# Performance work log

Measured on AMD Instinct MI355X. Metric: run time of the kernel, lower is better.

## Reference

```python
import jax, jax.numpy as jnp
import numpy as np

EPS = 1e-5
GROUPS = 32


def conv1x1(x, W, b):
    # x: (B,C,T), W: (O,C), b: (O,)
    return jnp.einsum('bct,oc->bot', x, W) + b[None, :, None]


def group_norm(x, gamma, beta):
    B, C, T = x.shape
    xg = x.reshape(B, GROUPS, (C // GROUPS) * T)
    mu = xg.mean(axis=-1, keepdims=True)
    var = xg.var(axis=-1, keepdims=True)
    xn = ((xg - mu) * jax.lax.rsqrt(var + EPS)).reshape(B, C, T)
    return xn * gamma[None, :, None] + beta[None, :, None]


def block(x, W, b, gamma, beta):
    return jax.nn.relu(group_norm(conv1x1(x, W, b), gamma, beta))


def setup_inputs() -> dict:
    key = jax.random.key(0)
    ks = jax.random.split(key, 8)
    B, C, P, T, TF = 4, 512, 512, 2048, 4096
    inp = {
        'feature': jax.random.normal(ks[0], (B, C, T), jnp.float32),
        'frame_level_feature': jax.random.uniform(ks[1], (B, C, TF), jnp.float32),
        # cur_point_conv: conv1x1 C->P + GN(32,P)
        'W1': jax.random.normal(ks[2], (P, C), jnp.float32) / np.sqrt(C),
        'b1': jnp.zeros((P,), jnp.float32),
        'g1': jnp.ones((P,), jnp.float32),
        'be1': jnp.zeros((P,), jnp.float32),
        # lr_conv: conv1x1 C->2P + GN(32,2P)
        'W2': jax.random.normal(ks[3], (2 * P, C), jnp.float32) / np.sqrt(C),
        'b2': jnp.zeros((2 * P,), jnp.float32),
        'g2': jnp.ones((2 * P,), jnp.float32),
        'be2': jnp.zeros((2 * P,), jnp.float32),
        # proposal_conv: conv1x1 4P->C + GN(32,C)
        'W3': jax.random.normal(ks[4], (C, 4 * P), jnp.float32) / np.sqrt(4 * P),
        'b3': jnp.zeros((C,), jnp.float32),
        'g3': jnp.ones((C,), jnp.float32),
        'be3': jnp.zeros((C,), jnp.float32),
    }
    return inp


def reference(feature, frame_level_feature, W1, b1, g1, be1, W2, b2, g2, be2, W3, b3, g3, be3):
    fm_short = block(feature, W1, b1, g1, be1)          # (B,P,T)
    feat = block(feature, W2, b2, g2, be2)              # (B,2P,T)
    t = feature.shape[2]
    # inverse-CDF resampling (uses batch 0 statistics, as original)
    mean_values = frame_level_feature.mean(axis=1)[0]   # (TF,)
    mean_values = mean_values / mean_values.sum()
    cdf = (jnp.cumsum(mean_values) * t).astype(jnp.int32)
    cdf = jnp.minimum(cdf, t - 1)                       # (TF,)
    # exact vectorization of findNearNum loop: first index with minimal |cdf-i|
    targets = jnp.arange(t, dtype=jnp.int32)
    idx = jnp.argmin(jnp.abs(cdf[None, :] - targets[:, None]), axis=1)  # (t,)
    sampled = frame_level_feature[:, :, idx]            # (B,C,t)
    mixed = jnp.concatenate([sampled, feat, fm_short], axis=1)  # (B,4P,t)
    mixed = block(mixed, W3, b3, g3, be3)               # (B,C,t)
    return (mixed, feat)
```

## Files before the change

kernel.cpp:

```cpp
#include <hip/hip_runtime.h>

typedef unsigned short u16;
typedef unsigned int   u32;
typedef __attribute__((ext_vector_type(8))) short short8;
typedef __attribute__((ext_vector_type(4))) short short4_t;
typedef __attribute__((ext_vector_type(4))) float f32x4;

__device__ __forceinline__ float bf2f(u16 v) {
  return __uint_as_float(((u32)v) << 16);
}
__device__ __forceinline__ u16 f2bf(float f) {
  u32 u = __float_as_uint(f);
  u32 r = (u + 0x7FFFu + ((u >> 16) & 1u)) >> 16;
  return (u16)r;
}
__device__ __forceinline__ float relu(float x) { return x < 0.f ? 0.f : x; }

__device__ __forceinline__ void gld16(const void* g, void* l) {
  __builtin_amdgcn_global_load_lds((const __attribute__((address_space(1))) u32*)g,
                                   (__attribute__((address_space(3))) u32*)l, 16, 0, 0);
}

__global__ void colmean_part_kernel(const float* __restrict__ frame,
                                    double* __restrict__ partD,
                                    float* __restrict__ rawZ) {
  if (blockIdx.x == 0 && blockIdx.y == 0 && threadIdx.x < 768)
    rawZ[threadIdx.x] = 0.f;
  int tf = blockIdx.x * 256 + threadIdx.x;
  int ch = blockIdx.y;
  const float* f0 = frame + tf + (size_t)ch * 64 * 4096;
  double s = 0.0;
  for (int c = 0; c < 64; ++c) s += (double)f0[(size_t)c * 4096];
  partD[ch * 4096 + tf] = s;
}

__global__ void scanD_kernel(const double* __restrict__ partD, int* __restrict__ cdf) {
  __shared__ double part[256];
  __shared__ double base[256];
  __shared__ double Ss;
  int tid = threadIdx.x;
  double loc[16];
  double s = 0.0;
#pragma unroll
  for (int i = 0; i < 16; ++i) {
    int tf = tid * 16 + i;
    double m = 0.0;
#pragma unroll
    for (int ch = 0; ch < 8; ++ch) m += partD[ch * 4096 + tf];
    loc[i] = m / 512.0;
    s += loc[i];
  }
  part[tid] = s;
  __syncthreads();
  if (tid == 0) {
    double t = 0.0;
    for (int i = 0; i < 256; ++i) t += part[i];
    Ss = t;
  }
  __syncthreads();
  double S = Ss;
  s = 0.0;
#pragma unroll
  for (int i = 0; i < 16; ++i) { loc[i] = loc[i] / S; s += loc[i]; }
  part[tid] = s;
  __syncthreads();
  if (tid == 0) {
    double c = 0.0;
    for (int i = 0; i < 256; ++i) { base[i] = c; c += part[i]; }
  }
  __syncthreads();
  double c = base[tid];
#pragma unroll
  for (int i = 0; i < 16; ++i) {
    c += loc[i];
    int iv = (int)(c * 2048.0);
    cdf[tid * 16 + i] = iv < 2047 ? iv : 2047;
  }
}

__global__ void argmin_kernel(const int* __restrict__ cdf, int* __restrict__ idx) {
  __shared__ int sd[256], sj[256];
  int target = blockIdx.x;
  int tid = threadIdx.x;
  int best = 0x7fffffff, bj = 0x7fffffff;
  for (int j = tid; j < 4096; j += 256) {
    int d = cdf[j] - target; d = d < 0 ? -d : d;
    if (d < best) { best = d; bj = j; }
  }
  sd[tid] = best; sj[tid] = bj;
  __syncthreads();
  for (int s = 128; s > 0; s >>= 1) {
    if (tid < s) {
      if (sd[tid+s] < sd[tid] || (sd[tid+s] == sd[tid] && sj[tid+s] < sj[tid])) {
        sd[tid] = sd[tid+s]; sj[tid] = sj[tid+s];
      }
    }
    __syncthreads();
  }
  if (tid == 0) idx[target] = sj[0];
}

__global__ void gatherTrans_kernel(const float* __restrict__ frame,
                                   const float* __restrict__ feature,
                                   const int* __restrict__ idx,
                                   u16* __restrict__ X3T, u16* __restrict__ featT) {
  __shared__ u16 tile[64][65];
  __shared__ int sidx[64];
  int cb = blockIdx.x * 64, t0 = blockIdx.y * 64;
  int b = blockIdx.z & 3, which = blockIdx.z >> 2;
  int tid = threadIdx.x;
  if (which == 0) {
    if (tid < 64) {
      int it = idx[t0 + tid];
      sidx[tid] = it < 0 ? 0 : (it > 4095 ? 4095 : it);
    }
    __syncthreads();
    const float* fb = frame + (size_t)b * 512 * 4096;
    for (int i = tid; i < 4096; i += 256) {
      int r = i >> 6, tt = i & 63;
      tile[tt][r] = f2bf(fb[(size_t)(cb + r) * 4096 + sidx[tt]]);
    }
    __syncthreads();
    u16* xb = X3T + (size_t)b * 2048 * 2048;
    for (int i = tid; i < 4096; i += 256) {
      int r = i >> 6, cc = i & 63;
      xb[(size_t)(t0 + r) * 2048 + cb + cc] = tile[r][cc];
    }
  } else {
    const float* xb = feature + (size_t)b * 512 * 2048;
    for (int i = tid; i < 4096; i += 256) {
      int r = i >> 6, tt = i & 63;
      tile[tt][r] = f2bf(xb[(size_t)(cb + r) * 2048 + t0 + tt]);
    }
    __syncthreads();
    u16* xtb = featT + (size_t)b * 2048 * 512;
    for (int i = tid; i < 4096; i += 256) {
      int r = i >> 6, cc = i & 63;
      xtb[(size_t)(t0 + r) * 512 + cb + cc] = tile[r][cc];
    }
  }
}

__global__ void convW12_kernel(const float* __restrict__ W1, const float* __restrict__ W2,
                               u16* __restrict__ dst) {
  int i = (blockIdx.x * 256 + threadIdx.x) * 4;
  f32x4 v = *(const f32x4*)(i < 262144 ? W1 + i : W2 + (i - 262144));
  short4_t o;
#pragma unroll
  for (int e = 0; e < 4; ++e) o[e] = (short)f2bf(v[e]);
  *(short4_t*)(dst + i) = o;
}
__global__ void convW_kernel(const float* __restrict__ src, u16* __restrict__ dst) {
  int i = (blockIdx.x * 256 + threadIdx.x) * 4;
  f32x4 v = *(const f32x4*)(src + i);
  short4_t o;
#pragma unroll
  for (int e = 0; e < 4; ++e) o[e] = (short)f2bf(v[e]);
  *(short4_t*)(dst + i) = o;
}

__global__ __launch_bounds__(128) void gemm12_kernel(
    const u16* __restrict__ A, const u16* __restrict__ Bt,
    const float* __restrict__ b1, const float* __restrict__ b2,
    float* __restrict__ Y, float* __restrict__ raw1, float* __restrict__ raw2)
{
  const int K = 512;
  __shared__ short As[2][2048];
  __shared__ short Bs[2][4096];
  const int tid = threadIdx.x;
  const int lane = tid & 63;
  const int w = tid >> 6;
  const int nt = blockIdx.x, mt = blockIdx.y, bb = blockIdx.z;
  const u16* Ab = A + (size_t)mt * 64 * K;
  const u16* Bb = Bt + ((size_t)bb * 2048 + (size_t)nt * 128) * K;
  const int lm = lane & 15, lq = lane >> 4;
  f32x4 acc[4][4] = {};

  auto stage = [&](int buf, int kt) {
#pragma unroll
    for (int p = 0; p < 2; ++p) {
      int chunk = tid + 128 * p;
      int row = chunk >> 2;
      int ko = ((chunk & 3) ^ ((row >> 1) & 3)) << 3;
      gld16(Ab + (size_t)row * K + kt + ko, (char*)As[buf] + chunk * 16);
    }
#pragma unroll
    for (int p = 0; p < 4; ++p) {
      int chunk = tid + 128 * p;
      int row = chunk >> 2;
      int ko = ((chunk & 3) ^ ((row >> 1) & 3)) << 3;
      gld16(Bb + (size_t)row * K + kt + ko, (char*)Bs[buf] + chunk * 16);
    }
  };

  stage(0, 0);
  for (int s = 0; s < 16; ++s) {
    int cur = s & 1;
    __syncthreads();
    if (s + 1 < 16) stage(cur ^ 1, (s + 1) << 5);
    short8 af[4], bfv[4];
#pragma unroll
    for (int i = 0; i < 4; ++i) {
      int r = i * 16 + lm;
      af[i] = *(const short8*)(As[cur] + r * 32 + ((lq ^ ((r >> 1) & 3)) << 3));
    }
#pragma unroll
    for (int j = 0; j < 4; ++j) {
      int r = w * 64 + j * 16 + lm;
      bfv[j] = *(const short8*)(Bs[cur] + r * 32 + ((lq ^ ((r >> 1) & 3)) << 3));
    }
#pragma unroll
    for (int i = 0; i < 4; ++i)
#pragma unroll
      for (int j = 0; j < 4; ++j)
        acc[i][j] = __builtin_amdgcn_mfma_f32_16x16x32_bf16(af[i], bfv[j], acc[i][j], 0, 0, 0);
  }

  float s1[4] = {0.f, 0.f, 0.f, 0.f};
  float s2[4] = {0.f, 0.f, 0.f, 0.f};
#pragma unroll
  for (int i = 0; i < 4; ++i) {
    int mbase = mt * 64 + i * 16 + lq * 4;
#pragma unroll
    for (int e = 0; e < 4; ++e) {
      int m = mbase + e;
      float bv = m < 512 ? b1[m] : b2[m - 512];
      float* yp = Y + ((size_t)bb * 1536 + m) * 2048 + nt * 128 + w * 64 + lm;
#pragma unroll
      for (int j = 0; j < 4; ++j) {
        float v = acc[i][j][e] + bv;
        yp[j * 16] = v;
        s1[i] += v; s2[i] += v * v;
      }
    }
  }
#pragma unroll
  for (int i = 0; i < 4; ++i) {
#pragma unroll
    for (int off = 32; off > 0; off >>= 1) {
      s1[i] += __shfl_xor(s1[i], off);
      s2[i] += __shfl_xor(s2[i], off);
    }
  }
  if (lane == 0) {
    if (mt < 8) {
#pragma unroll
      for (int i = 0; i < 4; ++i) {
        int g = mt * 4 + i;
        atomicAdd(&raw1[(bb * 32 + g) * 2],     s1[i]);
        atomicAdd(&raw1[(bb * 32 + g) * 2 + 1], s2[i]);
      }
    } else {
#pragma unroll
      for (int i = 0; i < 2; ++i) {
        int g = (mt - 8) * 2 + i;
        atomicAdd(&raw2[(bb * 32 + g) * 2],     s1[2 * i] + s1[2 * i + 1]);
        atomicAdd(&raw2[(bb * 32 + g) * 2 + 1], s2[2 * i] + s2[2 * i + 1]);
      }
    }
  }
}

__global__ __launch_bounds__(128) void gemm3s_kernel(
    const u16* __restrict__ A, const u16* __restrict__ Bt,
    const float* __restrict__ bias, float* __restrict__ Yp)
{
  const int K = 2048;
  __shared__ short As[2][2048];
  __shared__ short Bs[2][4096];
  const int tid = threadIdx.x;
  const int lane = tid & 63;
  const int w = tid >> 6;
  const int nt = blockIdx.x, mt = blockIdx.y;
  const int bb = blockIdx.z >> 1, ks = blockIdx.z & 1;
  const u16* Ab = A + (size_t)mt * 64 * K + ks * 1024;
  const u16* Bb = Bt + ((size_t)bb * 2048 + (size_t)nt * 128) * K + ks * 1024;
  const int lm = lane & 15, lq = lane >> 4;
  f32x4 acc[4][4] = {};

  auto stage = [&](int buf, int kt) {
#pragma unroll
    for (int p = 0; p < 2; ++p) {
      int chunk = tid + 128 * p;
      int row = chunk >> 2;
      int ko = ((chunk & 3) ^ ((row >> 1) & 3)) << 3;
      gld16(Ab + (size_t)row * K + kt + ko, (char*)As[buf] + chunk * 16);
    }
#pragma unroll
    for (int p = 0; p < 4; ++p) {
      int chunk = tid + 128 * p;
      int row = chunk >> 2;
      int ko = ((chunk & 3) ^ ((row >> 1) & 3)) << 3;
      gld16(Bb + (size_t)row * K + kt + ko, (char*)Bs[buf] + chunk * 16);
    }
  };

  stage(0, 0);
  for (int s = 0; s < 32; ++s) {
    int cur = s & 1;
    __syncthreads();
    if (s + 1 < 32) stage(cur ^ 1, (s + 1) << 5);
    short8 af[4], bfv[4];
#pragma unroll
    for (int i = 0; i < 4; ++i) {
      int r = i * 16 + lm;
      af[i] = *(const short8*)(As[cur] + r * 32 + ((lq ^ ((r >> 1) & 3)) << 3));
    }
#pragma unroll
    for (int j = 0; j < 4; ++j) {
      int r = w * 64 + j * 16 + lm;
      bfv[j] = *(const short8*)(Bs[cur] + r * 32 + ((lq ^ ((r >> 1) & 3)) << 3));
    }
#pragma unroll
    for (int i = 0; i < 4; ++i)
#pragma unroll
      for (int j = 0; j < 4; ++j)
        acc[i][j] = __builtin_amdgcn_mfma_f32_16x16x32_bf16(af[i], bfv[j], acc[i][j], 0, 0, 0);
  }
#pragma unroll
  for (int i = 0; i < 4; ++i) {
    int mbase = mt * 64 + i * 16 + lq * 4;
#pragma unroll
    for (int e = 0; e < 4; ++e) {
      int m = mbase + e;
      float bv = ks ? 0.f : bias[m];
      float* yp = Yp + ((size_t)(ks * 4 + bb) * 512 + m) * 2048 + nt * 128 + w * 64 + lm;
#pragma unroll
      for (int j = 0; j < 4; ++j)
        yp[j * 16] = acc[i][j][e] + bv;
    }
  }
}

__global__ void stats3p_kernel(const float* __restrict__ Yp, float* __restrict__ raw) {
  int chunk = blockIdx.x, g = blockIdx.y, b = blockIdx.z, tid = threadIdx.x;
  const f32x4* base = (const f32x4*)(Yp + ((size_t)b * 512 + g * 16) * 2048
                                        + (size_t)chunk * 4096);
  float s = 0.f, ss = 0.f;
#pragma unroll
  for (int i = 0; i < 4; ++i) {
    f32x4 a = base[tid + 256 * i];
    f32x4 c = base[tid + 256 * i + 1048576];
#pragma unroll
    for (int e = 0; e < 4; ++e) {
      float v = a[e] + c[e];
      s += v; ss += v * v;
    }
  }
  __shared__ float s1[256], s2[256];
  s1[tid] = s; s2[tid] = ss;
  __syncthreads();
  for (int st = 128; st > 0; st >>= 1) {
    if (tid < st) { s1[tid] += s1[tid + st]; s2[tid] += s2[tid + st]; }
    __syncthreads();
  }
  if (tid == 0) {
    atomicAdd(&raw[(b * 32 + g) * 2],     s1[0]);
    atomicAdd(&raw[(b * 32 + g) * 2 + 1], s2[0]);
  }
}

__global__ void normT12_kernel(const float* __restrict__ Y,
                               const float* __restrict__ raw1,
                               const float* __restrict__ raw2,
                               const float* __restrict__ g1, const float* __restrict__ be1,
                               const float* __restrict__ g2, const float* __restrict__ be2,
                               u16* __restrict__ X3T, float* __restrict__ featOut) {
  __shared__ u16 tile[64][65];
  int b = blockIdx.z, t0 = blockIdx.x * 64;
  int yb_idx = blockIdx.y;
  const int gn2 = yb_idx >= 8;
  int c0 = (gn2 ? yb_idx - 8 : yb_idx) * 64;
  const float* raw   = gn2 ? raw2 : raw1;
  const float* gamma = gn2 ? g2 : g1;
  const float* beta  = gn2 ? be2 : be1;
  const float inv_n  = gn2 ? (1.f / 65536.f) : (1.f / 32768.f);
  const int chBase   = gn2 ? 512 : 0;
  const int gShift   = gn2 ? 5 : 4;
  const int colBase  = gn2 ? 512 : 1536;
  const float* yb = Y + ((size_t)b * 1536 + chBase) * 2048;
  for (int i = threadIdx.x; i < 4096; i += 256) {
    int r = i >> 6, cc = i & 63;
    int ch = c0 + r;
    int gI = (b * 32 + (ch >> gShift)) * 2;
    float mu = raw[gI] * inv_n;
    float var = raw[gI + 1] * inv_n - mu * mu;
    float rs = 1.0f / sqrtf(var + 1e-5f);
    float v = yb[(size_t)ch * 2048 + t0 + cc];
    float o = relu((v - mu) * rs * gamma[ch] + beta[ch]);
    tile[cc][r] = f2bf(o);
    if (gn2) featOut[((size_t)b * 1024 + ch) * 2048 + t0 + cc] = o;
  }
  __syncthreads();
  for (int i = threadIdx.x; i < 4096; i += 256) {
    int r = i >> 6, cc = i & 63;
    X3T[((size_t)b * 2048 + t0 + r) * 2048 + colBase + c0 + cc] = tile[r][cc];
  }
}

__global__ void norm3_kernel(const float* __restrict__ Yp, const float* __restrict__ raw,
                             const float* __restrict__ gamma, const float* __restrict__ beta,
                             float* __restrict__ out) {
  int i4 = blockIdx.x * 256 + threadIdx.x;
  int b = i4 >> 18;
  int ch = (i4 >> 9) & 511;
  int gI = (b * 32 + (ch >> 4)) * 2;
  float mu = raw[gI] * (1.f / 32768.f);
  float var = raw[gI + 1] * (1.f / 32768.f) - mu * mu;
  float rs = 1.0f / sqrtf(var + 1e-5f);
  float ga = gamma[ch], bt = beta[ch];
  f32x4 a = ((const f32x4*)Yp)[i4];
  f32x4 c = ((const f32x4*)Yp)[i4 + 1048576];
  f32x4 o;
#pragma unroll
  for (int e = 0; e < 4; ++e)
    o[e] = relu((a[e] + c[e] - mu) * rs * ga + bt);
  ((f32x4*)out)[i4] = o;
}

extern "C" void kernel_launch(void* const* d_in, const int* in_sizes, int n_in,
                              void* d_out, int out_size, void* d_ws, size_t ws_size,
                              hipStream_t stream) {
  const float* feature = (const float*)d_in[0];
  const float* frame   = (const float*)d_in[1];
  const float* W1 = (const float*)d_in[2];
  const float* b1 = (const float*)d_in[3];
  const float* g1 = (const float*)d_in[4];
  const float* be1 = (const float*)d_in[5];
  const float* W2 = (const float*)d_in[6];
  const float* b2 = (const float*)d_in[7];
  const float* g2 = (const float*)d_in[8];
  const float* be2 = (const float*)d_in[9];
  const float* W3 = (const float*)d_in[10];
  const float* b3 = (const float*)d_in[11];
  const float* g3 = (const float*)d_in[12];
  const float* be3 = (const float*)d_in[13];

  char* ws = (char*)d_ws;
  u16*    X3T   = (u16*)(ws + 0);
  float*  Y12f  = (float*)(ws + 33554432);
  float*  Y3p   = (float*)(ws + 33554432);
  u16*    W3b   = (u16*)(ws + 67108864);
  double* partD = (double*)(ws + 50331648);
  u16*    featT = (u16*)(ws + 83886080);
  u16*    W12b  = (u16*)(ws + 92274688);
  int*    cdf   = (int*)(ws + 93847552);
  int*    idx   = (int*)(ws + 93863936);
  float*  raw1  = (float*)(ws + 93872128);
  float*  raw2  = (float*)(ws + 93873152);
  float*  raw3  = (float*)(ws + 93874176);

  float* outMixed = (float*)d_out;
  float* outFeat  = outMixed + (size_t)4 * 512 * 2048;

  colmean_part_kernel<<<dim3(16, 8), 256, 0, stream>>>(frame, partD, raw1);
  scanD_kernel<<<1, 256, 0, stream>>>(partD, cdf);
  argmin_kernel<<<2048, 256, 0, stream>>>(cdf, idx);
  gatherTrans_kernel<<<dim3(8, 32, 8), 256, 0, stream>>>(frame, feature, idx,
                                                         X3T, featT);
  convW12_kernel<<<768, 256, 0, stream>>>(W1, W2, W12b);
  gemm12_kernel<<<dim3(16, 24, 4), 128, 0, stream>>>(W12b, featT, b1, b2, Y12f,
                                                     raw1, raw2);
  normT12_kernel<<<dim3(32, 24, 4), 256, 0, stream>>>(Y12f, raw1, raw2,
                                                      g1, be1, g2, be2,
                                                      X3T, outFeat);
  convW_kernel<<<1024, 256, 0, stream>>>(W3, W3b);
  gemm3s_kernel<<<dim3(16, 8, 8), 128, 0, stream>>>(W3b, X3T, b3, Y3p);
  stats3p_kernel<<<dim3(8, 32, 4), 256, 0, stream>>>(Y3p, raw3);
  norm3_kernel<<<4096, 256, 0, stream>>>(Y3p, raw3, g3, be3, outMixed);
}
```

Measured before the change: 266.8 us.

## Fuse final GEMM split-K, GroupNorm stats and normalize via grid barrier

Replaces the split-K GEMM3 plus separate stats and normalize kernels with one kernel. Two 128-thread teams per block each handle half of K, combine partials through shared memory, and accumulate group statistics with warp shuffles and atomics. A software grid barrier over all 512 blocks then lets every block apply GroupNorm+ReLU from registers and write the output directly. This removes the round trip of the fp32 partial buffers through global memory, but it relies on all 512 blocks being co-resident for the spin barrier. The barrier counter is zeroed by extending the raw-stats reset in the first kernel.

```diff
diff --git a/kernel.cpp b/kernel.cpp
--- a/kernel.cpp
+++ b/kernel.cpp
@@ -24,8 +24,12 @@
 __global__ void colmean_part_kernel(const float* __restrict__ frame,
                                     double* __restrict__ partD,
                                     float* __restrict__ rawZ) {
-  if (blockIdx.x == 0 && blockIdx.y == 0 && threadIdx.x < 768)
+  if (blockIdx.x == 0 && blockIdx.y == 0) {
     rawZ[threadIdx.x] = 0.f;
+    rawZ[threadIdx.x + 256] = 0.f;
+    rawZ[threadIdx.x + 512] = 0.f;
+    rawZ[threadIdx.x + 768] = 0.f;
+  }
   int tf = blockIdx.x * 256 + threadIdx.x;
   int ch = blockIdx.y;
   const float* f0 = frame + tf + (size_t)ch * 64 * 4096;
@@ -261,37 +265,42 @@
   }
 }
 
-__global__ __launch_bounds__(128) void gemm3s_kernel(
+__global__ __launch_bounds__(256) void gemm3c_kernel(
     const u16* __restrict__ A, const u16* __restrict__ Bt,
-    const float* __restrict__ bias, float* __restrict__ Yp)
+    const float* __restrict__ bias,
+    const float* __restrict__ g3, const float* __restrict__ be3,
+    float* __restrict__ raw3, int* __restrict__ bar,
+    float* __restrict__ out)
 {
   const int K = 2048;
-  __shared__ short As[2][2048];
-  __shared__ short Bs[2][4096];
+  __shared__ char smem[49152];
   const int tid = threadIdx.x;
+  const int team = tid >> 7;
+  const int ttid = tid & 127;
   const int lane = tid & 63;
-  const int w = tid >> 6;
-  const int nt = blockIdx.x, mt = blockIdx.y;
-  const int bb = blockIdx.z >> 1, ks = blockIdx.z & 1;
-  const u16* Ab = A + (size_t)mt * 64 * K + ks * 1024;
-  const u16* Bb = Bt + ((size_t)bb * 2048 + (size_t)nt * 128) * K + ks * 1024;
+  const int w = (tid >> 6) & 1;
+  const int nt = blockIdx.x, mt = blockIdx.y, bb = blockIdx.z;
+  const u16* Ab = A + (size_t)mt * 64 * K + team * 1024;
+  const u16* Bb = Bt + ((size_t)bb * 2048 + (size_t)nt * 128) * K + team * 1024;
   const int lm = lane & 15, lq = lane >> 4;
+  short* As0 = (short*)(smem + team * 24576);
+  short* Bs0 = (short*)(smem + team * 24576 + 8192);
   f32x4 acc[4][4] = {};
 
   auto stage = [&](int buf, int kt) {
 #pragma unroll
     for (int p = 0; p < 2; ++p) {
-      int chunk = tid + 128 * p;
+      int chunk = ttid + 128 * p;
       int row = chunk >> 2;
       int ko = ((chunk & 3) ^ ((row >> 1) & 3)) << 3;
-      gld16(Ab + (size_t)row * K + kt + ko, (char*)As[buf] + chunk * 16);
+      gld16(Ab + (size_t)row * K + kt + ko, (char*)(As0 + buf * 2048) + chunk * 16);
     }
 #pragma unroll
     for (int p = 0; p < 4; ++p) {
-      int chunk = tid + 128 * p;
+      int chunk = ttid + 128 * p;
       int row = chunk >> 2;
       int ko = ((chunk & 3) ^ ((row >> 1) & 3)) << 3;
-      gld16(Bb + (size_t)row * K + kt + ko, (char*)Bs[buf] + chunk * 16);
+      gld16(Bb + (size_t)row * K + kt + ko, (char*)(Bs0 + buf * 4096) + chunk * 16);
     }
   };
 
@@ -300,16 +309,18 @@
     int cur = s & 1;
     __syncthreads();
     if (s + 1 < 32) stage(cur ^ 1, (s + 1) << 5);
+    const short* Asc = As0 + cur * 2048;
+    const short* Bsc = Bs0 + cur * 4096;
     short8 af[4], bfv[4];
 #pragma unroll
     for (int i = 0; i < 4; ++i) {
       int r = i * 16 + lm;
-      af[i] = *(const short8*)(As[cur] + r * 32 + ((lq ^ ((r >> 1) & 3)) << 3));
+      af[i] = *(const short8*)(Asc + r * 32 + ((lq ^ ((r >> 1) & 3)) << 3));
     }
 #pragma unroll
     for (int j = 0; j < 4; ++j) {
       int r = w * 64 + j * 16 + lm;
-      bfv[j] = *(const short8*)(Bs[cur] + r * 32 + ((lq ^ ((r >> 1) & 3)) << 3));
+      bfv[j] = *(const short8*)(Bsc + r * 32 + ((lq ^ ((r >> 1) & 3)) << 3));
     }
 #pragma unroll
     for (int i = 0; i < 4; ++i)
@@ -317,46 +328,86 @@
       for (int j = 0; j < 4; ++j)
         acc[i][j] = __builtin_amdgcn_mfma_f32_16x16x32_bf16(af[i], bfv[j], acc[i][j], 0, 0, 0);
   }
-#pragma unroll
-  for (int i = 0; i < 4; ++i) {
-    int mbase = mt * 64 + i * 16 + lq * 4;
-#pragma unroll
-    for (int e = 0; e < 4; ++e) {
-      int m = mbase + e;
-      float bv = ks ? 0.f : bias[m];
-      float* yp = Yp + ((size_t)(ks * 4 + bb) * 512 + m) * 2048 + nt * 128 + w * 64 + lm;
+
+  float* xch = (float*)smem;
+  __syncthreads();
+  if (team == 1) {
+#pragma unroll
+    for (int i = 0; i < 4; ++i)
 #pragma unroll
       for (int j = 0; j < 4; ++j)
-        yp[j * 16] = acc[i][j][e] + bv;
-    }
-  }
-}
-
-__global__ void stats3p_kernel(const float* __restrict__ Yp, float* __restrict__ raw) {
-  int chunk = blockIdx.x, g = blockIdx.y, b = blockIdx.z, tid = threadIdx.x;
-  const f32x4* base = (const f32x4*)(Yp + ((size_t)b * 512 + g * 16) * 2048
-                                        + (size_t)chunk * 4096);
-  float s = 0.f, ss = 0.f;
-#pragma unroll
-  for (int i = 0; i < 4; ++i) {
-    f32x4 a = base[tid + 256 * i];
-    f32x4 c = base[tid + 256 * i + 1048576];
-#pragma unroll
-    for (int e = 0; e < 4; ++e) {
-      float v = a[e] + c[e];
-      s += v; ss += v * v;
-    }
-  }
-  __shared__ float s1[256], s2[256];
-  s1[tid] = s; s2[tid] = ss;
-  __syncthreads();
-  for (int st = 128; st > 0; st >>= 1) {
-    if (tid < st) { s1[tid] += s1[tid + st]; s2[tid] += s2[tid + st]; }
-    __syncthreads();
-  }
+#pragma unroll
+        for (int e = 0; e < 4; ++e)
+          xch[(i * 16 + lq * 4 + e) * 130 + w * 64 + j * 16 + lm] = acc[i][j][e];
+  }
+  __syncthreads();
+
+  float s1[4] = {0.f, 0.f, 0.f, 0.f};
+  float s2[4] = {0.f, 0.f, 0.f, 0.f};
+  if (team == 0) {
+#pragma unroll
+    for (int i = 0; i < 4; ++i) {
+#pragma unroll
+      for (int e = 0; e < 4; ++e) {
+        float bv = bias[mt * 64 + i * 16 + lq * 4 + e];
+#pragma unroll
+        for (int j = 0; j < 4; ++j) {
+          float v = acc[i][j][e] + bv
+                  + xch[(i * 16 + lq * 4 + e) * 130 + w * 64 + j * 16 + lm];
+          acc[i][j][e] = v;
+          s1[i] += v; s2[i] += v * v;
+        }
+      }
+    }
+#pragma unroll
+    for (int i = 0; i < 4; ++i) {
+#pragma unroll
+      for (int off = 32; off > 0; off >>= 1) {
+        s1[i] += __shfl_xor(s1[i], off);
+        s2[i] += __shfl_xor(s2[i], off);
+      }
+    }
+    if (lane == 0) {
+#pragma unroll
+      for (int i = 0; i < 4; ++i) {
+        int g = mt * 4 + i;
+        atomicAdd(&raw3[(bb * 32 + g) * 2],     s1[i]);
+        atomicAdd(&raw3[(bb * 32 + g) * 2 + 1], s2[i]);
+      }
+      __threadfence();
+    }
+  }
+
+  __syncthreads();
   if (tid == 0) {
-    atomicAdd(&raw[(b * 32 + g) * 2],     s1[0]);
-    atomicAdd(&raw[(b * 32 + g) * 2 + 1], s2[0]);
+    __hip_atomic_fetch_add(bar, 1, __ATOMIC_RELEASE, __HIP_MEMORY_SCOPE_AGENT);
+    while (__hip_atomic_load(bar, __ATOMIC_ACQUIRE, __HIP_MEMORY_SCOPE_AGENT) < 512) {
+      __builtin_amdgcn_s_sleep(8);
+    }
+  }
+  __syncthreads();
+
+  if (team == 0) {
+    float v = 0.f;
+    if (lane < 8)
+      v = __hip_atomic_load(&raw3[(bb * 32 + mt * 4 + (lane >> 1)) * 2 + (lane & 1)],
+                            __ATOMIC_RELAXED, __HIP_MEMORY_SCOPE_AGENT);
+#pragma unroll
+    for (int i = 0; i < 4; ++i) {
+      float sA = __shfl(v, i * 2);
+      float sB = __shfl(v, i * 2 + 1);
+      float mu = sA * (1.f / 32768.f);
+      float rs = 1.0f / sqrtf(sB * (1.f / 32768.f) - mu * mu + 1e-5f);
+#pragma unroll
+      for (int e = 0; e < 4; ++e) {
+        int m = mt * 64 + i * 16 + lq * 4 + e;
+        float ga = g3[m], bt = be3[m];
+        float* yp = out + ((size_t)bb * 512 + m) * 2048 + nt * 128 + w * 64 + lm;
+#pragma unroll
+        for (int j = 0; j < 4; ++j)
+          yp[j * 16] = relu((acc[i][j][e] - mu) * rs * ga + bt);
+      }
+    }
   }
 }
 
@@ -398,26 +449,6 @@
   }
 }
 
-__global__ void norm3_kernel(const float* __restrict__ Yp, const float* __restrict__ raw,
-                             const float* __restrict__ gamma, const float* __restrict__ beta,
-                             float* __restrict__ out) {
-  int i4 = blockIdx.x * 256 + threadIdx.x;
-  int b = i4 >> 18;
-  int ch = (i4 >> 9) & 511;
-  int gI = (b * 32 + (ch >> 4)) * 2;
-  float mu = raw[gI] * (1.f / 32768.f);
-  float var = raw[gI + 1] * (1.f / 32768.f) - mu * mu;
-  float rs = 1.0f / sqrtf(var + 1e-5f);
-  float ga = gamma[ch], bt = beta[ch];
-  f32x4 a = ((const f32x4*)Yp)[i4];
-  f32x4 c = ((const f32x4*)Yp)[i4 + 1048576];
-  f32x4 o;
-#pragma unroll
-  for (int e = 0; e < 4; ++e)
-    o[e] = relu((a[e] + c[e] - mu) * rs * ga + bt);
-  ((f32x4*)out)[i4] = o;
-}
-
 extern "C" void kernel_launch(void* const* d_in, const int* in_sizes, int n_in,
                               void* d_out, int out_size, void* d_ws, size_t ws_size,
                               hipStream_t stream) {
@@ -439,7 +470,6 @@
   char* ws = (char*)d_ws;
   u16*    X3T   = (u16*)(ws + 0);
   float*  Y12f  = (float*)(ws + 33554432);
-  float*  Y3p   = (float*)(ws + 33554432);
   u16*    W3b   = (u16*)(ws + 67108864);
   double* partD = (double*)(ws + 50331648);
   u16*    featT = (u16*)(ws + 83886080);
@@ -449,6 +479,7 @@
   float*  raw1  = (float*)(ws + 93872128);
   float*  raw2  = (float*)(ws + 93873152);
   float*  raw3  = (float*)(ws + 93874176);
+  int*    bar   = (int*)(ws + 93875200);
 
   float* outMixed = (float*)d_out;
   float* outFeat  = outMixed + (size_t)4 * 512 * 2048;
@@ -465,7 +496,6 @@
                                                       g1, be1, g2, be2,
                                                       X3T, outFeat);
   convW_kernel<<<1024, 256, 0, stream>>>(W3, W3b);
-  gemm3s_kernel<<<dim3(16, 8, 8), 128, 0, stream>>>(W3b, X3T, b3, Y3p);
-  stats3p_kernel<<<dim3(8, 32, 4), 256, 0, stream>>>(Y3p, raw3);
-  norm3_kernel<<<4096, 256, 0, stream>>>(Y3p, raw3, g3, be3, outMixed);
-}
+  gemm3c_kernel<<<dim3(16, 8, 4), 256, 0, stream>>>(W3b, X3T, b3, g3, be3,
+                                                    raw3, bar, outMixed);
+}
```

Result: slower. 308.9 us (+15.7%).

## Fuse GN3 stats and normalization via grid barrier; merge W12 conversion into gather

Applied to the files above, without the earlier changes.

Replaces the separate stats3p and norm3 kernels with one kernel. Each block loads its slice of the split-K partials once, keeps the sums in registers, and contributes group sums via atomics. A device-wide spin barrier then lets every block read the final statistics and normalise. This avoids re-reading Y3p and removes one launch. It also folds the W1/W2 bf16 conversion into extra z-slices of the gather kernel, and zeroes 1024 floats so the barrier counter is reset each call. The barrier assumes all 1024 blocks are co-resident, which risks deadlock if occupancy does not allow that.

```diff
diff --git a/kernel.cpp b/kernel.cpp
--- a/kernel.cpp
+++ b/kernel.cpp
@@ -24,8 +24,12 @@
 __global__ void colmean_part_kernel(const float* __restrict__ frame,
                                     double* __restrict__ partD,
                                     float* __restrict__ rawZ) {
-  if (blockIdx.x == 0 && blockIdx.y == 0 && threadIdx.x < 768)
+  if (blockIdx.x == 0 && blockIdx.y == 0) {
     rawZ[threadIdx.x] = 0.f;
+    rawZ[threadIdx.x + 256] = 0.f;
+    rawZ[threadIdx.x + 512] = 0.f;
+    rawZ[threadIdx.x + 768] = 0.f;
+  }
   int tf = blockIdx.x * 256 + threadIdx.x;
   int ch = blockIdx.y;
   const float* f0 = frame + tf + (size_t)ch * 64 * 4096;
@@ -103,12 +107,26 @@
 __global__ void gatherTrans_kernel(const float* __restrict__ frame,
                                    const float* __restrict__ feature,
                                    const int* __restrict__ idx,
-                                   u16* __restrict__ X3T, u16* __restrict__ featT) {
+                                   const float* __restrict__ W1,
+                                   const float* __restrict__ W2,
+                                   u16* __restrict__ X3T, u16* __restrict__ featT,
+                                   u16* __restrict__ W12b) {
   __shared__ u16 tile[64][65];
   __shared__ int sidx[64];
+  int tid = threadIdx.x;
+  int zz = blockIdx.z;
+  if (zz >= 8) {
+    int flat = (zz - 8) * 256 + blockIdx.y * 8 + blockIdx.x;
+    int i = (flat * 256 + tid) * 4;
+    f32x4 v = *(const f32x4*)(i < 262144 ? W1 + i : W2 + (i - 262144));
+    short4_t o;
+#pragma unroll
+    for (int e = 0; e < 4; ++e) o[e] = (short)f2bf(v[e]);
+    *(short4_t*)(W12b + i) = o;
+    return;
+  }
   int cb = blockIdx.x * 64, t0 = blockIdx.y * 64;
-  int b = blockIdx.z & 3, which = blockIdx.z >> 2;
-  int tid = threadIdx.x;
+  int b = zz & 3, which = zz >> 2;
   if (which == 0) {
     if (tid < 64) {
       int it = idx[t0 + tid];
@@ -141,15 +159,6 @@
   }
 }
 
-__global__ void convW12_kernel(const float* __restrict__ W1, const float* __restrict__ W2,
-                               u16* __restrict__ dst) {
-  int i = (blockIdx.x * 256 + threadIdx.x) * 4;
-  f32x4 v = *(const f32x4*)(i < 262144 ? W1 + i : W2 + (i - 262144));
-  short4_t o;
-#pragma unroll
-  for (int e = 0; e < 4; ++e) o[e] = (short)f2bf(v[e]);
-  *(short4_t*)(dst + i) = o;
-}
 __global__ void convW_kernel(const float* __restrict__ src, u16* __restrict__ dst) {
   int i = (blockIdx.x * 256 + threadIdx.x) * 4;
   f32x4 v = *(const f32x4*)(src + i);
@@ -329,34 +338,6 @@
       for (int j = 0; j < 4; ++j)
         yp[j * 16] = acc[i][j][e] + bv;
     }
-  }
-}
-
-__global__ void stats3p_kernel(const float* __restrict__ Yp, float* __restrict__ raw) {
-  int chunk = blockIdx.x, g = blockIdx.y, b = blockIdx.z, tid = threadIdx.x;
-  const f32x4* base = (const f32x4*)(Yp + ((size_t)b * 512 + g * 16) * 2048
-                                        + (size_t)chunk * 4096);
-  float s = 0.f, ss = 0.f;
-#pragma unroll
-  for (int i = 0; i < 4; ++i) {
-    f32x4 a = base[tid + 256 * i];
-    f32x4 c = base[tid + 256 * i + 1048576];
-#pragma unroll
-    for (int e = 0; e < 4; ++e) {
-      float v = a[e] + c[e];
-      s += v; ss += v * v;
-    }
-  }
-  __shared__ float s1[256], s2[256];
-  s1[tid] = s; s2[tid] = ss;
-  __syncthreads();
-  for (int st = 128; st > 0; st >>= 1) {
-    if (tid < st) { s1[tid] += s1[tid + st]; s2[tid] += s2[tid + st]; }
-    __syncthreads();
-  }
-  if (tid == 0) {
-    atomicAdd(&raw[(b * 32 + g) * 2],     s1[0]);
-    atomicAdd(&raw[(b * 32 + g) * 2 + 1], s2[0]);
   }
 }
 
@@ -398,24 +379,73 @@
   }
 }
 
-__global__ void norm3_kernel(const float* __restrict__ Yp, const float* __restrict__ raw,
-                             const float* __restrict__ gamma, const float* __restrict__ beta,
-                             float* __restrict__ out) {
-  int i4 = blockIdx.x * 256 + threadIdx.x;
-  int b = i4 >> 18;
-  int ch = (i4 >> 9) & 511;
-  int gI = (b * 32 + (ch >> 4)) * 2;
-  float mu = raw[gI] * (1.f / 32768.f);
-  float var = raw[gI + 1] * (1.f / 32768.f) - mu * mu;
-  float rs = 1.0f / sqrtf(var + 1e-5f);
-  float ga = gamma[ch], bt = beta[ch];
-  f32x4 a = ((const f32x4*)Yp)[i4];
-  f32x4 c = ((const f32x4*)Yp)[i4 + 1048576];
-  f32x4 o;
-#pragma unroll
-  for (int e = 0; e < 4; ++e)
-    o[e] = relu((a[e] + c[e] - mu) * rs * ga + bt);
-  ((f32x4*)out)[i4] = o;
+__global__ __launch_bounds__(256) void norm3f_kernel(
+    const float* __restrict__ Yp,
+    const float* __restrict__ gamma, const float* __restrict__ beta,
+    float* __restrict__ raw3, int* __restrict__ bar,
+    float* __restrict__ out)
+{
+  const int tid = threadIdx.x;
+  const int blk = blockIdx.x;
+  const int b = blk >> 8;
+  const int ch0 = (blk & 255) * 2;
+  const int g = ch0 >> 4;
+  const size_t base4 = (size_t)blk * 1024;
+  const f32x4* yp4 = (const f32x4*)Yp;
+
+  f32x4 v[4];
+  float s = 0.f, ss = 0.f;
+#pragma unroll
+  for (int k = 0; k < 4; ++k) {
+    size_t i4 = base4 + tid + 256 * k;
+    f32x4 a = yp4[i4];
+    f32x4 c = yp4[i4 + 1048576];
+#pragma unroll
+    for (int e = 0; e < 4; ++e) {
+      float x = a[e] + c[e];
+      v[k][e] = x;
+      s += x; ss += x * x;
+    }
+  }
+  __shared__ float s1[256], s2[256];
+  __shared__ float stat[2];
+  s1[tid] = s; s2[tid] = ss;
+  __syncthreads();
+  for (int st = 128; st > 0; st >>= 1) {
+    if (tid < st) { s1[tid] += s1[tid + st]; s2[tid] += s2[tid + st]; }
+    __syncthreads();
+  }
+  if (tid == 0) {
+    atomicAdd(&raw3[(b * 32 + g) * 2],     s1[0]);
+    atomicAdd(&raw3[(b * 32 + g) * 2 + 1], s2[0]);
+    __threadfence();
+    __hip_atomic_fetch_add(bar, 1, __ATOMIC_RELEASE, __HIP_MEMORY_SCOPE_AGENT);
+    while (__hip_atomic_load(bar, __ATOMIC_ACQUIRE, __HIP_MEMORY_SCOPE_AGENT) < 1024) {
+      __builtin_amdgcn_s_sleep(8);
+    }
+    float sA = __hip_atomic_load(&raw3[(b * 32 + g) * 2],     __ATOMIC_RELAXED,
+                                 __HIP_MEMORY_SCOPE_AGENT);
+    float sB = __hip_atomic_load(&raw3[(b * 32 + g) * 2 + 1], __ATOMIC_RELAXED,
+                                 __HIP_MEMORY_SCOPE_AGENT);
+    float mu = sA * (1.f / 32768.f);
+    stat[0] = mu;
+    stat[1] = 1.0f / sqrtf(sB * (1.f / 32768.f) - mu * mu + 1e-5f);
+  }
+  __syncthreads();
+  const float mu = stat[0], rs = stat[1];
+  const float ga0 = gamma[ch0], bt0 = beta[ch0];
+  const float ga1 = gamma[ch0 + 1], bt1 = beta[ch0 + 1];
+  f32x4* out4 = (f32x4*)out;
+#pragma unroll
+  for (int k = 0; k < 4; ++k) {
+    float ga = k < 2 ? ga0 : ga1;
+    float bt = k < 2 ? bt0 : bt1;
+    f32x4 o;
+#pragma unroll
+    for (int e = 0; e < 4; ++e)
+      o[e] = relu((v[k][e] - mu) * rs * ga + bt);
+    out4[base4 + tid + 256 * k] = o;
+  }
 }
 
 extern "C" void kernel_launch(void* const* d_in, const int* in_sizes, int n_in,
@@ -449,6 +479,7 @@
   float*  raw1  = (float*)(ws + 93872128);
   float*  raw2  = (float*)(ws + 93873152);
   float*  raw3  = (float*)(ws + 93874176);
+  int*    bar   = (int*)(ws + 93875200);
 
   float* outMixed = (float*)d_out;
   float* outFeat  = outMixed + (size_t)4 * 512 * 2048;
@@ -456,9 +487,8 @@
   colmean_part_kernel<<<dim3(16, 8), 256, 0, stream>>>(frame, partD, raw1);
   scanD_kernel<<<1, 256, 0, stream>>>(partD, cdf);
   argmin_kernel<<<2048, 256, 0, stream>>>(cdf, idx);
-  gatherTrans_kernel<<<dim3(8, 32, 8), 256, 0, stream>>>(frame, feature, idx,
-                                                         X3T, featT);
-  convW12_kernel<<<768, 256, 0, stream>>>(W1, W2, W12b);
+  gatherTrans_kernel<<<dim3(8, 32, 11), 256, 0, stream>>>(frame, feature, idx,
+                                                          W1, W2, X3T, featT, W12b);
   gemm12_kernel<<<dim3(16, 24, 4), 128, 0, stream>>>(W12b, featT, b1, b2, Y12f,
                                                      raw1, raw2);
   normT12_kernel<<<dim3(32, 24, 4), 256, 0, stream>>>(Y12f, raw1, raw2,
@@ -466,6 +496,5 @@
                                                       X3T, outFeat);
   convW_kernel<<<1024, 256, 0, stream>>>(W3, W3b);
   gemm3s_kernel<<<dim3(16, 8, 8), 128, 0, stream>>>(W3b, X3T, b3, Y3p);
-  stats3p_kernel<<<dim3(8, 32, 4), 256, 0, stream>>>(Y3p, raw3);
-  norm3_kernel<<<4096, 256, 0, stream>>>(Y3p, raw3, g3, be3, outMixed);
-}
+  norm3f_kernel<<<1024, 256, 0, stream>>>(Y3p, g3, be3, raw3, bar, outMixed);
+}
```

New measurement: 362.7 us. 35.9% more time.

## Replace brute-force argmin with binary search on monotone CDF and fuse weight conversion

Applied to the files above, without the earlier changes.

Replaces the 2048-block brute-force argmin kernel with a binary search over the monotone CDF, computed inline inside the gather/transpose kernel. The W1/W2 bf16 conversion is also folded into the same launch as extra z-slices, removing two kernel launches. The search relies on the CDF being non-decreasing, which holds because the inputs are cumulative sums of positive means. Its tie-breaking is meant to reproduce the first-minimal-index rule.

```diff
diff --git a/kernel.cpp b/kernel.cpp
--- a/kernel.cpp
+++ b/kernel.cpp
@@ -24,8 +24,11 @@
 __global__ void colmean_part_kernel(const float* __restrict__ frame,
                                     double* __restrict__ partD,
                                     float* __restrict__ rawZ) {
-  if (blockIdx.x == 0 && blockIdx.y == 0 && threadIdx.x < 768)
+  if (blockIdx.x == 0 && blockIdx.y == 0) {
     rawZ[threadIdx.x] = 0.f;
+    rawZ[threadIdx.x + 256] = 0.f;
+    rawZ[threadIdx.x + 512] = 0.f;
+  }
   int tf = blockIdx.x * 256 + threadIdx.x;
   int ch = blockIdx.y;
   const float* f0 = frame + tf + (size_t)ch * 64 * 4096;
@@ -78,42 +81,45 @@
   }
 }
 
-__global__ void argmin_kernel(const int* __restrict__ cdf, int* __restrict__ idx) {
-  __shared__ int sd[256], sj[256];
-  int target = blockIdx.x;
-  int tid = threadIdx.x;
-  int best = 0x7fffffff, bj = 0x7fffffff;
-  for (int j = tid; j < 4096; j += 256) {
-    int d = cdf[j] - target; d = d < 0 ? -d : d;
-    if (d < best) { best = d; bj = j; }
-  }
-  sd[tid] = best; sj[tid] = bj;
-  __syncthreads();
-  for (int s = 128; s > 0; s >>= 1) {
-    if (tid < s) {
-      if (sd[tid+s] < sd[tid] || (sd[tid+s] == sd[tid] && sj[tid+s] < sj[tid])) {
-        sd[tid] = sd[tid+s]; sj[tid] = sj[tid+s];
-      }
-    }
-    __syncthreads();
-  }
-  if (tid == 0) idx[target] = sj[0];
+__device__ __forceinline__ int lowbound(const int* __restrict__ cdf, int hi0, int v) {
+  int lo = 0, hi = hi0;
+  while (lo < hi) { int mid = (lo + hi) >> 1; if (cdf[mid] < v) lo = mid + 1; else hi = mid; }
+  return lo;
+}
+__device__ __forceinline__ int argmin_cdf(const int* __restrict__ cdf, int t) {
+  int j2 = lowbound(cdf, 4096, t);
+  if (j2 == 0) return 0;
+  if (j2 == 4096) return lowbound(cdf, 4096, cdf[4095]);
+  int d2 = cdf[j2] - t, d1 = t - cdf[j2 - 1];
+  if (d2 < d1) return j2;
+  return lowbound(cdf, j2, cdf[j2 - 1]);
 }
 
 __global__ void gatherTrans_kernel(const float* __restrict__ frame,
                                    const float* __restrict__ feature,
-                                   const int* __restrict__ idx,
-                                   u16* __restrict__ X3T, u16* __restrict__ featT) {
+                                   const int* __restrict__ cdf,
+                                   const float* __restrict__ W1,
+                                   const float* __restrict__ W2,
+                                   u16* __restrict__ X3T, u16* __restrict__ featT,
+                                   u16* __restrict__ W12b) {
   __shared__ u16 tile[64][65];
   __shared__ int sidx[64];
+  int tid = threadIdx.x;
+  int zz = blockIdx.z;
+  if (zz >= 8) {
+    int flat = (zz - 8) * 256 + blockIdx.y * 8 + blockIdx.x;
+    int i = (flat * 256 + tid) * 4;
+    f32x4 v = *(const f32x4*)(i < 262144 ? W1 + i : W2 + (i - 262144));
+    short4_t o;
+#pragma unroll
+    for (int e = 0; e < 4; ++e) o[e] = (short)f2bf(v[e]);
+    *(short4_t*)(W12b + i) = o;
+    return;
+  }
   int cb = blockIdx.x * 64, t0 = blockIdx.y * 64;
-  int b = blockIdx.z & 3, which = blockIdx.z >> 2;
-  int tid = threadIdx.x;
+  int b = zz & 3, which = zz >> 2;
   if (which == 0) {
-    if (tid < 64) {
-      int it = idx[t0 + tid];
-      sidx[tid] = it < 0 ? 0 : (it > 4095 ? 4095 : it);
-    }
+    if (tid < 64) sidx[tid] = argmin_cdf(cdf, t0 + tid);
     __syncthreads();
     const float* fb = frame + (size_t)b * 512 * 4096;
     for (int i = tid; i < 4096; i += 256) {
@@ -141,15 +147,6 @@
   }
 }
 
-__global__ void convW12_kernel(const float* __restrict__ W1, const float* __restrict__ W2,
-                               u16* __restrict__ dst) {
-  int i = (blockIdx.x * 256 + threadIdx.x) * 4;
-  f32x4 v = *(const f32x4*)(i < 262144 ? W1 + i : W2 + (i - 262144));
-  short4_t o;
-#pragma unroll
-  for (int e = 0; e < 4; ++e) o[e] = (short)f2bf(v[e]);
-  *(short4_t*)(dst + i) = o;
-}
 __global__ void convW_kernel(const float* __restrict__ src, u16* __restrict__ dst) {
   int i = (blockIdx.x * 256 + threadIdx.x) * 4;
   f32x4 v = *(const f32x4*)(src + i);
@@ -445,7 +442,6 @@
   u16*    featT = (u16*)(ws + 83886080);
   u16*    W12b  = (u16*)(ws + 92274688);
   int*    cdf   = (int*)(ws + 93847552);
-  int*    idx   = (int*)(ws + 93863936);
   float*  raw1  = (float*)(ws + 93872128);
   float*  raw2  = (float*)(ws + 93873152);
   float*  raw3  = (float*)(ws + 93874176);
@@ -455,10 +451,8 @@
 
   colmean_part_kernel<<<dim3(16, 8), 256, 0, stream>>>(frame, partD, raw1);
   scanD_kernel<<<1, 256, 0, stream>>>(partD, cdf);
-  argmin_kernel<<<2048, 256, 0, stream>>>(cdf, idx);
-  gatherTrans_kernel<<<dim3(8, 32, 8), 256, 0, stream>>>(frame, feature, idx,
-                                                         X3T, featT);
-  convW12_kernel<<<768, 256, 0, stream>>>(W1, W2, W12b);
+  gatherTrans_kernel<<<dim3(8, 32, 11), 256, 0, stream>>>(frame, feature, cdf,
+                                                          W1, W2, X3T, featT, W12b);
   gemm12_kernel<<<dim3(16, 24, 4), 128, 0, stream>>>(W12b, featT, b1, b2, Y12f,
                                                      raw1, raw2);
   normT12_kernel<<<dim3(32, 24, 4), 256, 0, stream>>>(Y12f, raw1, raw2,
```

Result: faster. 258.4 us (-3.2%).
